# Kernel tuning notes

Hardware: AMD Instinct MI355X
Metric: run time of the kernel (lower is better)

Reference implementation:

```python
import jax, jax.numpy as jnp
import numpy as np
import itertools as itt

N_FEATURES = 12
ORDER = 3
EPS = 1e-5  # torch BatchNorm1d default


def _mask_flat_idx(order: int, n_features: int) -> np.ndarray:
    # Faithful port of PolynomialExpansion._create_mask: keep entries whose
    # coords are nondecreasing (unique monomials) and not all-zero (no constant).
    n1 = n_features + 1
    mask = np.ones(order * (n1,), dtype=bool)
    for coords in itt.product(*(range(n1) for _ in range(order))):
        if sum(coords) == 0:
            mask[coords] = False
        for k in range(order - 1):
            if coords[k + 1] < coords[k]:
                mask[coords] = False
                break
    return np.nonzero(mask.ravel())[0]


IDX = jnp.asarray(_mask_flat_idx(ORDER, N_FEATURES))  # [454] static monomial indices
N_EXPANDED = int(IDX.shape[0])  # 454 = C(15,3) - 1


def setup_inputs() -> dict:
    key = jax.random.key(0)
    k1, k2, k3 = jax.random.split(key, 3)
    x = jax.random.normal(k1, (65536, N_FEATURES), dtype=jnp.float32)
    # BatchNorm1d affine parameters (torch inits to 1/0; perturb for non-trivial grads)
    bn_weight = 1.0 + 0.1 * jax.random.normal(k2, (N_EXPANDED,), dtype=jnp.float32)
    bn_bias = 0.1 * jax.random.normal(k3, (N_EXPANDED,), dtype=jnp.float32)
    return {"x": x, "bn_weight": bn_weight, "bn_bias": bn_bias}


def reference(x, bn_weight, bn_bias):
    B = x.shape[0]
    n1 = N_FEATURES + 1
    # y = [1, x] -> [B, 13]
    y = jnp.concatenate([jnp.ones((B, 1), dtype=x.dtype), x], axis=-1)
    # Dense outer-product tensor m[b, i0, ..., i_{order-1}] = prod_k y[b, i_k]
    yy = y
    m = y
    for _ in range(ORDER - 1):
        yy = yy[..., None]          # [B, 13, 1(, 1...)]
        m = m[:, None, ...] * yy    # grows to [B, 13, 13(, 13...)]
    # Gather unique monomials (mask over the last `order` dims, flattened)
    feats = m.reshape(B, -1)[:, IDX]  # [B, 454]
    # BatchNorm1d in training mode: batch mean, biased batch var
    mean = jnp.mean(feats, axis=0)
    var = jnp.mean(jnp.square(feats - mean), axis=0)
    return (feats - mean) * jax.lax.rsqrt(var + EPS) * bn_weight + bn_bias
```

## Files before the change

### kernel.cpp

```cpp
#include <hip/hip_runtime.h>

#define NF 13
#define NEXP 454
#define NROWS 65536
#define BN_EPS 1e-5f
#define SBLK 512
#define SROWS (NROWS / SBLK)
#define PARTW 908
#define SPAD (SROWS + 4)
#define WROWS 64
#define WPAD (WROWS + 4)

__device__ __forceinline__ void decode_triple(int j, int& i0, int& i1, int& i2) {
    int g = j + 1;
    i0 = 0;
    for (;;) {
        int m = NF - i0;
        int c = m * (m + 1) / 2;
        if (g < c) break;
        g -= c; ++i0;
    }
    i1 = i0;
    for (;;) {
        int m = NF - i1;
        if (g < m) break;
        g -= m; ++i1;
    }
    i2 = i1 + g;
}

__global__ __launch_bounds__(256) void stats_kernel(const float* __restrict__ x,
                                                    float* __restrict__ part) {
    __shared__ float yc[NF][SPAD];
    const int tid = threadIdx.x;
    const int row0 = blockIdx.x * SROWS;

    for (int idx = tid; idx < SROWS * 12; idx += 256) {
        int r = idx / 12, c = idx - r * 12;
        yc[c + 1][r] = x[(size_t)row0 * 12 + idx];
    }
    for (int r = tid; r < SROWS; r += 256) yc[0][r] = 1.0f;
    __syncthreads();

    const int j0 = tid;
    const int j1 = tid + 256;
    const bool has1 = (j1 < NEXP);
    int a0, a1, a2, b0 = 0, b1 = 0, b2 = 0;
    decode_triple(j0, a0, a1, a2);
    if (has1) decode_triple(j1, b0, b1, b2);

    float s0 = 0.f, q0 = 0.f, s1 = 0.f, q1 = 0.f;
    for (int r = 0; r < SROWS; r += 4) {
        float4 va = *reinterpret_cast<const float4*>(&yc[a0][r]);
        float4 vb = *reinterpret_cast<const float4*>(&yc[a1][r]);
        float4 vc = *reinterpret_cast<const float4*>(&yc[a2][r]);
        float f;
        f = va.x * vb.x * vc.x; s0 += f; q0 += f * f;
        f = va.y * vb.y * vc.y; s0 += f; q0 += f * f;
        f = va.z * vb.z * vc.z; s0 += f; q0 += f * f;
        f = va.w * vb.w * vc.w; s0 += f; q0 += f * f;
        if (has1) {
            float4 wa = *reinterpret_cast<const float4*>(&yc[b0][r]);
            float4 wb = *reinterpret_cast<const float4*>(&yc[b1][r]);
            float4 wc = *reinterpret_cast<const float4*>(&yc[b2][r]);
            f = wa.x * wb.x * wc.x; s1 += f; q1 += f * f;
            f = wa.y * wb.y * wc.y; s1 += f; q1 += f * f;
            f = wa.z * wb.z * wc.z; s1 += f; q1 += f * f;
            f = wa.w * wb.w * wc.w; s1 += f; q1 += f * f;
        }
    }
    float* p = part + (size_t)blockIdx.x * PARTW;
    p[j0] = s0;
    p[NEXP + j0] = q0;
    if (has1) {
        p[j1] = s1;
        p[NEXP + j1] = q1;
    }
}

#define FIN_FPB 32
__global__ __launch_bounds__(256) void finalize_kernel(const float* __restrict__ part,
                                                       const float* __restrict__ w,
                                                       const float* __restrict__ b,
                                                       float* __restrict__ ss) {
    __shared__ float reds[8][FIN_FPB];
    __shared__ float redq[8][FIN_FPB];
    const int fl = threadIdx.x & 31;
    const int k  = threadIdx.x >> 5;
    const int f  = blockIdx.x * FIN_FPB + fl;
    float s = 0.f, q = 0.f;
    if (f < NEXP) {
        #pragma unroll 4
        for (int i = 0; i < SBLK / 8; ++i) {
            const float* p = part + (size_t)(k * (SBLK / 8) + i) * PARTW;
            s += p[f];
            q += p[NEXP + f];
        }
    }
    reds[k][fl] = s;
    redq[k][fl] = q;
    __syncthreads();
    if (threadIdx.x < FIN_FPB && f < NEXP) {
        float ts = 0.f, tq = 0.f;
        #pragma unroll
        for (int kk = 0; kk < 8; ++kk) { ts += reds[kk][fl]; tq += redq[kk][fl]; }
        const float inv_n = 1.0f / (float)NROWS;
        float mean = ts * inv_n;
        float var  = tq * inv_n - mean * mean;
        float scale = rsqrtf(var + BN_EPS) * w[f];
        ss[f] = scale;
        ss[NEXP + f] = b[f] - mean * scale;
    }
}

__global__ __launch_bounds__(256) void write_kernel(const float* __restrict__ x,
                                                    const float* __restrict__ ss,
                                                    float* __restrict__ out) {
    __shared__ float yc[NF][WPAD];
    const int tid = threadIdx.x;
    const int row0 = blockIdx.x * WROWS;

    for (int idx = tid; idx < WROWS * 12; idx += 256) {
        int r = idx / 12, c = idx - r * 12;
        yc[c + 1][r] = x[(size_t)row0 * 12 + idx];
    }
    for (int r = tid; r < WROWS; r += 256) yc[0][r] = 1.0f;

    const int j0 = tid;
    const int j1 = tid + 256;
    const bool has1 = (j1 < NEXP);
    int a0, a1, a2, b0 = 0, b1 = 0, b2 = 0;
    decode_triple(j0, a0, a1, a2);
    if (has1) decode_triple(j1, b0, b1, b2);
    const float sc0 = ss[j0], sh0 = ss[NEXP + j0];
    const float sc1 = has1 ? ss[j1] : 0.f, sh1 = has1 ? ss[NEXP + j1] : 0.f;
    __syncthreads();

    for (int r = 0; r < WROWS; r += 4) {
        float4 va = *reinterpret_cast<const float4*>(&yc[a0][r]);
        float4 vb = *reinterpret_cast<const float4*>(&yc[a1][r]);
        float4 vc = *reinterpret_cast<const float4*>(&yc[a2][r]);
        float* o = out + (size_t)(row0 + r) * NEXP + j0;
        o[0 * NEXP] = va.x * vb.x * vc.x * sc0 + sh0;
        o[1 * NEXP] = va.y * vb.y * vc.y * sc0 + sh0;
        o[2 * NEXP] = va.z * vb.z * vc.z * sc0 + sh0;
        o[3 * NEXP] = va.w * vb.w * vc.w * sc0 + sh0;
        if (has1) {
            float4 wa = *reinterpret_cast<const float4*>(&yc[b0][r]);
            float4 wb = *reinterpret_cast<const float4*>(&yc[b1][r]);
            float4 wc = *reinterpret_cast<const float4*>(&yc[b2][r]);
            float* o1 = out + (size_t)(row0 + r) * NEXP + j1;
            o1[0 * NEXP] = wa.x * wb.x * wc.x * sc1 + sh1;
            o1[1 * NEXP] = wa.y * wb.y * wc.y * sc1 + sh1;
            o1[2 * NEXP] = wa.z * wb.z * wc.z * sc1 + sh1;
            o1[3 * NEXP] = wa.w * wb.w * wc.w * sc1 + sh1;
        }
    }
}

extern "C" void kernel_launch(void* const* d_in, const int* in_sizes, int n_in,
                              void* d_out, int out_size, void* d_ws, size_t ws_size,
                              hipStream_t stream) {
    const float* x  = (const float*)d_in[0];
    const float* bw = (const float*)d_in[1];
    const float* bb = (const float*)d_in[2];
    float* out  = (float*)d_out;
    float* part = (float*)d_ws;
    float* ss   = part + (size_t)SBLK * PARTW;

    stats_kernel<<<SBLK, 256, 0, stream>>>(x, part);
    finalize_kernel<<<(NEXP + FIN_FPB - 1) / FIN_FPB, 256, 0, stream>>>(part, bw, bb, ss);
    write_kernel<<<NROWS / WROWS, 256, 0, stream>>>(x, ss, out);
}
```

Measured before the change: 44.96 us.

## Fuse stats, finalize and write into one persistent kernel with grid barriers

```diff
diff --git a/kernel.cpp b/kernel.cpp
--- a/kernel.cpp
+++ b/kernel.cpp
@@ -4,12 +4,11 @@
 #define NEXP 454
 #define NROWS 65536
 #define BN_EPS 1e-5f
-#define SBLK 512
-#define SROWS (NROWS / SBLK)
+#define NBLK 512
+#define BROWS (NROWS / NBLK)
 #define PARTW 908
-#define SPAD (SROWS + 4)
-#define WROWS 64
-#define WPAD (WROWS + 4)
+#define SPAD (BROWS + 4)
+#define FIN_FPB 32
 
 __device__ __forceinline__ void decode_triple(int j, int& i0, int& i1, int& i2) {
     int g = j + 1;
@@ -29,17 +28,43 @@
     i2 = i1 + g;
 }
 
-__global__ __launch_bounds__(256) void stats_kernel(const float* __restrict__ x,
-                                                    float* __restrict__ part) {
+__device__ __forceinline__ void grid_bar(int* ctr, int n) {
+    __syncthreads();
+    if (threadIdx.x == 0) {
+        __threadfence();
+        __hip_atomic_fetch_add(ctr, 1, __ATOMIC_ACQ_REL, __HIP_MEMORY_SCOPE_AGENT);
+        while (__hip_atomic_load(ctr, __ATOMIC_ACQUIRE, __HIP_MEMORY_SCOPE_AGENT) < n) {
+            __builtin_amdgcn_s_sleep(2);
+        }
+        __threadfence();
+    }
+    __syncthreads();
+}
+
+__global__ void zero_ctr_kernel(int* __restrict__ ctr) {
+    if (threadIdx.x < 2) ctr[threadIdx.x] = 0;
+}
+
+__global__ __launch_bounds__(256, 2) void fused_kernel(
+        const float* __restrict__ x,
+        const float* __restrict__ w,
+        const float* __restrict__ b,
+        float* __restrict__ part,
+        float* __restrict__ ss,
+        int* __restrict__ ctr,
+        float* __restrict__ out) {
     __shared__ float yc[NF][SPAD];
+    __shared__ float reds[8][FIN_FPB];
+    __shared__ float redq[8][FIN_FPB];
     const int tid = threadIdx.x;
-    const int row0 = blockIdx.x * SROWS;
+    const int blk = blockIdx.x;
+    const int row0 = blk * BROWS;
 
-    for (int idx = tid; idx < SROWS * 12; idx += 256) {
+    for (int idx = tid; idx < BROWS * 12; idx += 256) {
         int r = idx / 12, c = idx - r * 12;
         yc[c + 1][r] = x[(size_t)row0 * 12 + idx];
     }
-    for (int r = tid; r < SROWS; r += 256) yc[0][r] = 1.0f;
+    for (int r = tid; r < BROWS; r += 256) yc[0][r] = 1.0f;
     __syncthreads();
 
     const int j0 = tid;
@@ -50,7 +75,7 @@
     if (has1) decode_triple(j1, b0, b1, b2);
 
     float s0 = 0.f, q0 = 0.f, s1 = 0.f, q1 = 0.f;
-    for (int r = 0; r < SROWS; r += 4) {
+    for (int r = 0; r < BROWS; r += 4) {
         float4 va = *reinterpret_cast<const float4*>(&yc[a0][r]);
         float4 vb = *reinterpret_cast<const float4*>(&yc[a1][r]);
         float4 vc = *reinterpret_cast<const float4*>(&yc[a2][r]);
@@ -69,74 +94,53 @@
             f = wa.w * wb.w * wc.w; s1 += f; q1 += f * f;
         }
     }
-    float* p = part + (size_t)blockIdx.x * PARTW;
-    p[j0] = s0;
-    p[NEXP + j0] = q0;
-    if (has1) {
-        p[j1] = s1;
-        p[NEXP + j1] = q1;
-    }
-}
-
-#define FIN_FPB 32
-__global__ __launch_bounds__(256) void finalize_kernel(const float* __restrict__ part,
-                                                       const float* __restrict__ w,
-                                                       const float* __restrict__ b,
-                                                       float* __restrict__ ss) {
-    __shared__ float reds[8][FIN_FPB];
-    __shared__ float redq[8][FIN_FPB];
-    const int fl = threadIdx.x & 31;
-    const int k  = threadIdx.x >> 5;
-    const int f  = blockIdx.x * FIN_FPB + fl;
-    float s = 0.f, q = 0.f;
-    if (f < NEXP) {
-        #pragma unroll 4
-        for (int i = 0; i < SBLK / 8; ++i) {
-            const float* p = part + (size_t)(k * (SBLK / 8) + i) * PARTW;
-            s += p[f];
-            q += p[NEXP + f];
+    {
+        float* p = part + (size_t)blk * PARTW;
+        p[j0] = s0;
+        p[NEXP + j0] = q0;
+        if (has1) {
+            p[j1] = s1;
+            p[NEXP + j1] = q1;
         }
     }
-    reds[k][fl] = s;
-    redq[k][fl] = q;
-    __syncthreads();
-    if (threadIdx.x < FIN_FPB && f < NEXP) {
-        float ts = 0.f, tq = 0.f;
-        #pragma unroll
-        for (int kk = 0; kk < 8; ++kk) { ts += reds[kk][fl]; tq += redq[kk][fl]; }
-        const float inv_n = 1.0f / (float)NROWS;
-        float mean = ts * inv_n;
-        float var  = tq * inv_n - mean * mean;
-        float scale = rsqrtf(var + BN_EPS) * w[f];
-        ss[f] = scale;
-        ss[NEXP + f] = b[f] - mean * scale;
+
+    grid_bar(&ctr[0], NBLK);
+
+    if (blk < (NEXP + FIN_FPB - 1) / FIN_FPB) {
+        const int fl = tid & 31;
+        const int k  = tid >> 5;
+        const int f  = blk * FIN_FPB + fl;
+        float s = 0.f, q = 0.f;
+        if (f < NEXP) {
+            #pragma unroll 4
+            for (int i = 0; i < NBLK / 8; ++i) {
+                const float* p = part + (size_t)(k * (NBLK / 8) + i) * PARTW;
+                s += p[f];
+                q += p[NEXP + f];
+            }
+        }
+        reds[k][fl] = s;
+        redq[k][fl] = q;
+        __syncthreads();
+        if (tid < FIN_FPB && f < NEXP) {
+            float ts = 0.f, tq = 0.f;
+            #pragma unroll
+            for (int kk = 0; kk < 8; ++kk) { ts += reds[kk][fl]; tq += redq[kk][fl]; }
+            const float inv_n = 1.0f / (float)NROWS;
+            float mean = ts * inv_n;
+            float var  = tq * inv_n - mean * mean;
+            float scale = rsqrtf(var + BN_EPS) * w[f];
+            ss[f] = scale;
+            ss[NEXP + f] = b[f] - mean * scale;
+        }
     }
-}
 
-__global__ __launch_bounds__(256) void write_kernel(const float* __restrict__ x,
-                                                    const float* __restrict__ ss,
-                                                    float* __restrict__ out) {
-    __shared__ float yc[NF][WPAD];
-    const int tid = threadIdx.x;
-    const int row0 = blockIdx.x * WROWS;
+    grid_bar(&ctr[1], NBLK);
 
-    for (int idx = tid; idx < WROWS * 12; idx += 256) {
-        int r = idx / 12, c = idx - r * 12;
-        yc[c + 1][r] = x[(size_t)row0 * 12 + idx];
-    }
-    for (int r = tid; r < WROWS; r += 256) yc[0][r] = 1.0f;
-
-    const int j0 = tid;
-    const int j1 = tid + 256;
-    const bool has1 = (j1 < NEXP);
-    int a0, a1, a2, b0 = 0, b1 = 0, b2 = 0;
-    decode_triple(j0, a0, a1, a2);
-    if (has1) decode_triple(j1, b0, b1, b2);
     const float sc0 = ss[j0], sh0 = ss[NEXP + j0];
     const float sc1 = has1 ? ss[j1] : 0.f, sh1 = has1 ? ss[NEXP + j1] : 0.f;
-    __syncthreads();
 
-    for (int r = 0; r < WROWS; r += 4) {
+    for (int r = 0; r < BROWS; r += 4) {
         float4 va = *reinterpret_cast<const float4*>(&yc[a0][r]);
         float4 vb = *reinterpret_cast<const float4*>(&yc[a1][r]);
         float4 vc = *reinterpret_cast<const float4*>(&yc[a2][r]);
@@ -166,9 +170,9 @@
     const float* bb = (const float*)d_in[2];
     float* out  = (float*)d_out;
     float* part = (float*)d_ws;
-    float* ss   = part + (size_t)SBLK * PARTW;
+    float* ss   = part + (size_t)NBLK * PARTW;
+    int*   ctr  = (int*)(ss + 2 * NEXP);
 
-    stats_kernel<<<SBLK, 256, 0, stream>>>(x, part);
-    finalize_kernel<<<(NEXP + FIN_FPB - 1) / FIN_FPB, 256, 0, stream>>>(part, bw, bb, ss);
-    write_kernel<<<NROWS / WROWS, 256, 0, stream>>>(x, ss, out);
+    zero_ctr_kernel<<<1, 64, 0, stream>>>(ctr);
+    fused_kernel<<<NBLK, 256, 0, stream>>>(x, bw, bb, part, ss, ctr, out);
 }
```

Result: slower. 153.5 us (+241.4%).
